# Kernel tuning notes

Measured on AMD Instinct MI355X. Metric: run time of the kernel, lower is better.

The kernel has to match this reference:

```python
import jax, jax.numpy as jnp
import numpy as np

HEADS = 16
HEAD_DIM = 4  # attention_channels(64) // num_heads(16)


def setup_inputs() -> dict:
    key = jax.random.key(0)
    ks = jax.random.split(key, 9)
    C, AC = 256, 64
    N, H, W = 1, 64, 64
    s_in = 1.0 / np.sqrt(C)
    s_out = 1.0 / np.sqrt(AC)
    return {
        "X":  jax.random.normal(ks[0], (N, C, H, W), jnp.float32),
        "Wq": jax.random.normal(ks[1], (AC, C), jnp.float32) * s_in,
        "bq": jax.random.normal(ks[2], (AC,), jnp.float32) * 0.01,
        "Wk": jax.random.normal(ks[3], (AC, C), jnp.float32) * s_in,
        "bk": jax.random.normal(ks[4], (AC,), jnp.float32) * 0.01,
        "Wv": jax.random.normal(ks[5], (AC, C), jnp.float32) * s_in,
        "bv": jax.random.normal(ks[6], (AC,), jnp.float32) * 0.01,
        "Wo": jax.random.normal(ks[7], (C, AC), jnp.float32) * s_out,
        "bo": jax.random.normal(ks[8], (C,), jnp.float32) * 0.01,
    }


def _l2norm_over_dim(x, eps=1e-12):
    # torch F.normalize(dim=-2): x / max(||x||_2, eps) along head-dim axis
    n = jnp.sqrt(jnp.sum(x * x, axis=-2, keepdims=True))
    return x / jnp.maximum(n, eps)


def reference(X, Wq, bq, Wk, bk, Wv, bv, Wo, bo):
    N, C, H, W = X.shape
    L = H * W
    def proj(Wm, bm):
        # 1x1 conv == channel matmul; reshape to (N, heads, d, L)
        y = jnp.einsum('oc,nchw->nohw', Wm, X) + bm[None, :, None, None]
        return y.reshape(N, HEADS, HEAD_DIM, L)
    Q = _l2norm_over_dim(proj(Wq, bq))
    K = _l2norm_over_dim(proj(Wk, bk))
    V = proj(Wv, bv)
    # attention_weights[l, m] = q_l . k_m, softmax over m (rows)
    A = jax.nn.softmax(jnp.einsum('nhdl,nhdm->nhlm', Q, K), axis=-1)
    # faithful to original: out = V @ A  -> out[d, i] = sum_j V[d, j] * A[j, i]
    out = jnp.einsum('nhdj,nhji->nhdi', V, A)
    out = out.reshape(N, HEADS * HEAD_DIM, H, W)
    out = jnp.einsum('co,nohw->nchw', Wo, out) + bo[None, :, None, None]
    return out + X
```

## Files before the change

### kernel.cpp

```cpp
#include <hip/hip_runtime.h>
#include <math.h>


constexpr int SL = 4096;
constexpr int NF = 126;

__device__ __forceinline__ float invfact(int e) {
    return e < 2 ? 1.f : e == 2 ? 0.5f : e == 3 ? (1.f / 6.f)
         : e == 4 ? (1.f / 24.f) : (1.f / 120.f);
}
__device__ __forceinline__ void f2abcd(int f, int& A, int& B, int& C, int& D) {
    for (int a = 0; a <= 5; ++a)
        for (int b = 0; b <= 5 - a; ++b)
            for (int c = 0; c <= 5 - a - b; ++c)
                for (int d = 0; d <= 5 - a - b - c; ++d)
                    if (f-- == 0) { A = a; B = b; C = c; D = d; return; }
}

#define FOR_MONOMIALS(BODY)                         \
    {                                               \
        int f = 0;                                  \
        _Pragma("unroll")                           \
        for (int a = 0; a <= 5; ++a)                \
        _Pragma("unroll")                           \
        for (int b = 0; b <= 5 - a; ++b)            \
        _Pragma("unroll")                           \
        for (int c = 0; c <= 5 - a - b; ++c)        \
        _Pragma("unroll")                           \
        for (int d = 0; d <= 5 - a - b - c; ++d) {  \
            BODY;                                   \
            ++f;                                    \
        }                                           \
    }

#define BUILD_POWERS(q)                                   \
    float p0[6], p1[6], p2[6], p3[6];                     \
    p0[0] = p1[0] = p2[0] = p3[0] = 1.f;                  \
    _Pragma("unroll")                                     \
    for (int t_ = 1; t_ < 6; ++t_) {                      \
        p0[t_] = p0[t_ - 1] * (q).x; p1[t_] = p1[t_ - 1] * (q).y; \
        p2[t_] = p2[t_ - 1] * (q).z; p3[t_] = p3[t_ - 1] * (q).w; }

__global__ __launch_bounds__(256) void qkv_kernel(
    const float* __restrict__ X,
    const float* __restrict__ Wq, const float* __restrict__ bq,
    const float* __restrict__ Wk, const float* __restrict__ bk,
    const float* __restrict__ Wv, const float* __restrict__ bv,
    float* __restrict__ Qn, float* __restrict__ Kn, float* __restrict__ V4)
{
    const int tid  = threadIdx.x;
    const int lane = tid & 63;
    const int wv   = __builtin_amdgcn_readfirstlane(tid >> 6);
    const int lt   = blockIdx.x;
    const int rb   = blockIdx.y;
    const int type = rb >> 2;
    const int rit  = (rb & 3) * 16 + wv * 4;
    const int l    = lt * 64 + lane;

    const float* W = type == 0 ? Wq : type == 1 ? Wk : Wv;
    const float* B = type == 0 ? bq : type == 1 ? bk : bv;
    const float* w0 = W + (rit + 0) * 256;
    const float* w1 = W + (rit + 1) * 256;
    const float* w2 = W + (rit + 2) * 256;
    const float* w3 = W + (rit + 3) * 256;

    float y0 = B[rit + 0], y1 = B[rit + 1], y2 = B[rit + 2], y3 = B[rit + 3];
    const float* Xl = X + l;
    #pragma unroll 8
    for (int c = 0; c < 256; ++c) {
        float x = Xl[c * SL];
        y0 = fmaf(w0[c], x, y0);
        y1 = fmaf(w1[c], x, y1);
        y2 = fmaf(w2[c], x, y2);
        y3 = fmaf(w3[c], x, y3);
    }
    if (type < 2) {
        float n = sqrtf(y0*y0 + y1*y1 + y2*y2 + y3*y3);
        float inv = 1.f / fmaxf(n, 1e-12f);
        y0 *= inv; y1 *= inv; y2 *= inv; y3 *= inv;
    }
    const int h = rit >> 2;
    float* base = type == 0 ? Qn : type == 1 ? Kn : V4;
    ((float4*)base)[h * SL + l] = make_float4(y0, y1, y2, y3);
}

template <int FC>
__device__ __forceinline__ void psi_accum(int h, int jc, int tid,
        const float* __restrict__ Kn, float acc[8])
{
    for (int u = 0; u < 4; ++u) {
        int j = jc * 1024 + u * 256 + tid;
        float4 k = ((const float4*)Kn)[h * SL + j];
        BUILD_POWERS(k)
        FOR_MONOMIALS({
            if (f >= FC * 8 && f < FC * 8 + 8)
                acc[f - FC * 8] += (p0[a] * p1[b]) * (p2[c] * p3[d]);
        })
    }
}

__global__ __launch_bounds__(256) void ssum_kernel(
    const float* __restrict__ Kn, float* __restrict__ Sp)
{
    const int tid = threadIdx.x;
    const int fc  = blockIdx.x;
    const int h   = blockIdx.y;
    const int jc  = blockIdx.z;
    float acc[8];
    #pragma unroll
    for (int k = 0; k < 8; ++k) acc[k] = 0.f;
    switch (fc) {
        case 0:  psi_accum<0 >(h, jc, tid, Kn, acc); break;
        case 1:  psi_accum<1 >(h, jc, tid, Kn, acc); break;
        case 2:  psi_accum<2 >(h, jc, tid, Kn, acc); break;
        case 3:  psi_accum<3 >(h, jc, tid, Kn, acc); break;
        case 4:  psi_accum<4 >(h, jc, tid, Kn, acc); break;
        case 5:  psi_accum<5 >(h, jc, tid, Kn, acc); break;
        case 6:  psi_accum<6 >(h, jc, tid, Kn, acc); break;
        case 7:  psi_accum<7 >(h, jc, tid, Kn, acc); break;
        case 8:  psi_accum<8 >(h, jc, tid, Kn, acc); break;
        case 9:  psi_accum<9 >(h, jc, tid, Kn, acc); break;
        case 10: psi_accum<10>(h, jc, tid, Kn, acc); break;
        case 11: psi_accum<11>(h, jc, tid, Kn, acc); break;
        case 12: psi_accum<12>(h, jc, tid, Kn, acc); break;
        case 13: psi_accum<13>(h, jc, tid, Kn, acc); break;
        case 14: psi_accum<14>(h, jc, tid, Kn, acc); break;
        default: psi_accum<15>(h, jc, tid, Kn, acc); break;
    }
    #pragma unroll
    for (int off = 32; off; off >>= 1)
        #pragma unroll
        for (int k = 0; k < 8; ++k) acc[k] += __shfl_down(acc[k], off);
    __shared__ float red[4][8];
    const int lane = tid & 63, wv = tid >> 6;
    if (lane == 0) {
        #pragma unroll
        for (int k = 0; k < 8; ++k) red[wv][k] = acc[k];
    }
    __syncthreads();
    if (tid < 8) {
        int f = fc * 8 + tid;
        if (f < NF) {
            float s = (red[0][tid] + red[1][tid]) + (red[2][tid] + red[3][tid]);
            int A, B, C, D; f2abcd(f, A, B, C, D);
            Sp[(jc * 16 + h) * 128 + f] =
                s * ((invfact(A) * invfact(B)) * (invfact(C) * invfact(D)));
        }
    }
}

__global__ __launch_bounds__(256) void zvz_kernel(
    const float* __restrict__ Qn, const float* __restrict__ Sp,
    const float* __restrict__ V4, float* __restrict__ Vz)
{
    __shared__ float Sf[128];
    const int tid = threadIdx.x;
    const int h   = blockIdx.y;
    if (tid < 128) {
        float s = 0.f;
        #pragma unroll
        for (int jc = 0; jc < 4; ++jc) s += Sp[(jc * 16 + h) * 128 + tid];
        Sf[tid] = s;
    }
    __syncthreads();
    const int j = blockIdx.x * 256 + tid;
    float4 q = ((const float4*)Qn)[h * SL + j];
    BUILD_POWERS(q)
    float z = 0.f;
    FOR_MONOMIALS({ z = fmaf((p0[a]*p1[b])*(p2[c]*p3[d]), Sf[f], z); })
    float inv = 1.f / z;
    float4 v = ((const float4*)V4)[h * SL + j];
    ((float4*)Vz)[h * SL + j] = make_float4(v.x*inv, v.y*inv, v.z*inv, v.w*inv);
}

template <int FC>
__device__ __forceinline__ void m_accum(int h, int jc, int tid,
        const float* __restrict__ Qn, const float* __restrict__ Vz,
        float acc[32])
{
    for (int u = 0; u < 4; ++u) {
        int j = jc * 1024 + u * 256 + tid;
        float4 q = ((const float4*)Qn)[h * SL + j];
        float4 v = ((const float4*)Vz)[h * SL + j];
        BUILD_POWERS(q)
        FOR_MONOMIALS({
            if (f >= FC * 8 && f < FC * 8 + 8) {
                const int fi = f - FC * 8;
                float m = (p0[a] * p1[b]) * (p2[c] * p3[d]);
                acc[fi*4+0] = fmaf(m, v.x, acc[fi*4+0]);
                acc[fi*4+1] = fmaf(m, v.y, acc[fi*4+1]);
                acc[fi*4+2] = fmaf(m, v.z, acc[fi*4+2]);
                acc[fi*4+3] = fmaf(m, v.w, acc[fi*4+3]);
            }
        })
    }
}

__global__ __launch_bounds__(256) void mmat_kernel(
    const float* __restrict__ Qn, const float* __restrict__ Vz,
    float* __restrict__ Mp)
{
    const int tid = threadIdx.x;
    const int fc  = blockIdx.x;
    const int h   = blockIdx.y;
    const int jc  = blockIdx.z;
    float acc[32];
    #pragma unroll
    for (int k = 0; k < 32; ++k) acc[k] = 0.f;
    switch (fc) {
        case 0:  m_accum<0 >(h, jc, tid, Qn, Vz, acc); break;
        case 1:  m_accum<1 >(h, jc, tid, Qn, Vz, acc); break;
        case 2:  m_accum<2 >(h, jc, tid, Qn, Vz, acc); break;
        case 3:  m_accum<3 >(h, jc, tid, Qn, Vz, acc); break;
        case 4:  m_accum<4 >(h, jc, tid, Qn, Vz, acc); break;
        case 5:  m_accum<5 >(h, jc, tid, Qn, Vz, acc); break;
        case 6:  m_accum<6 >(h, jc, tid, Qn, Vz, acc); break;
        case 7:  m_accum<7 >(h, jc, tid, Qn, Vz, acc); break;
        case 8:  m_accum<8 >(h, jc, tid, Qn, Vz, acc); break;
        case 9:  m_accum<9 >(h, jc, tid, Qn, Vz, acc); break;
        case 10: m_accum<10>(h, jc, tid, Qn, Vz, acc); break;
        case 11: m_accum<11>(h, jc, tid, Qn, Vz, acc); break;
        case 12: m_accum<12>(h, jc, tid, Qn, Vz, acc); break;
        case 13: m_accum<13>(h, jc, tid, Qn, Vz, acc); break;
        case 14: m_accum<14>(h, jc, tid, Qn, Vz, acc); break;
        default: m_accum<15>(h, jc, tid, Qn, Vz, acc); break;
    }
    #pragma unroll
    for (int off = 32; off; off >>= 1)
        #pragma unroll
        for (int k = 0; k < 32; ++k) acc[k] += __shfl_down(acc[k], off);
    __shared__ float red[4][32];
    const int lane = tid & 63, wv = tid >> 6;
    if (lane == 0) {
        #pragma unroll
        for (int k = 0; k < 32; ++k) red[wv][k] = acc[k];
    }
    __syncthreads();
    if (tid < 32) {
        int fi = tid >> 2, dd = tid & 3;
        int f = fc * 8 + fi;
        if (f < NF) {
            float s = (red[0][tid] + red[1][tid]) + (red[2][tid] + red[3][tid]);
            int A, B, C, D; f2abcd(f, A, B, C, D);
            s *= (invfact(A) * invfact(B)) * (invfact(C) * invfact(D));
            Mp[((jc * 16 + h) * 128 + f) * 4 + dd] = s;
        }
    }
}

template <int FC>
__device__ __forceinline__ void ao_accum(
        const float p0[6], const float p1[6], const float p2[6],
        const float p3[6], const float4* __restrict__ Mc, float acc[4])
{
    FOR_MONOMIALS({
        if (f >= FC * 32 && f < FC * 32 + 32 && f < NF) {
            float m = (p0[a] * p1[b]) * (p2[c] * p3[d]);
            float4 mm = Mc[f - FC * 32];
            acc[0] = fmaf(m, mm.x, acc[0]); acc[1] = fmaf(m, mm.y, acc[1]);
            acc[2] = fmaf(m, mm.z, acc[2]); acc[3] = fmaf(m, mm.w, acc[3]);
        }
    })
}

__global__ __launch_bounds__(256) void ao_kernel(
    const float* __restrict__ Kn, const float* __restrict__ Mp,
    float* __restrict__ AOp)
{
    __shared__ __align__(16) float Mc[32 * 4];
    const int tid = threadIdx.x;
    const int h   = blockIdx.y;
    const int fc  = blockIdx.z;
    const int nfl = (fc == 3) ? 30 : 32;
    if (tid < nfl * 4) {
        int fi = tid >> 2, dd = tid & 3;
        int f = fc * 32 + fi;
        float s = 0.f;
        #pragma unroll
        for (int jc = 0; jc < 4; ++jc)
            s += Mp[((jc * 16 + h) * 128 + f) * 4 + dd];
        Mc[fi * 4 + dd] = s;
    } else if (tid < 128) {
        Mc[tid] = 0.f;
    }
    __syncthreads();

    const int i = blockIdx.x * 256 + tid;
    float4 k = ((const float4*)Kn)[h * SL + i];
    BUILD_POWERS(k)
    float acc[4] = {0.f, 0.f, 0.f, 0.f};
    switch (fc) {
        case 0:  ao_accum<0>(p0, p1, p2, p3, (const float4*)Mc, acc); break;
        case 1:  ao_accum<1>(p0, p1, p2, p3, (const float4*)Mc, acc); break;
        case 2:  ao_accum<2>(p0, p1, p2, p3, (const float4*)Mc, acc); break;
        default: ao_accum<3>(p0, p1, p2, p3, (const float4*)Mc, acc); break;
    }
    float* A = AOp + (size_t)fc * 64 * SL;
    A[(h * 4 + 0) * SL + i] = acc[0];
    A[(h * 4 + 1) * SL + i] = acc[1];
    A[(h * 4 + 2) * SL + i] = acc[2];
    A[(h * 4 + 3) * SL + i] = acc[3];
}

__global__ __launch_bounds__(256) void oproj_kernel(
    const float* __restrict__ AOp, const float* __restrict__ Wo,
    const float* __restrict__ bo, const float* __restrict__ X,
    float* __restrict__ Y)
{
    const int lane = threadIdx.x & 63;
    const int wv   = __builtin_amdgcn_readfirstlane(threadIdx.x >> 6);
    const int i    = blockIdx.x * 64 + lane;
    const int cb   = blockIdx.y * 16 + wv * 4;

    float a0 = 0.f, a1 = 0.f, a2 = 0.f, a3 = 0.f;
    #pragma unroll 8
    for (int o = 0; o < 64; ++o) {
        float x = (AOp[o * SL + i] + AOp[262144 + o * SL + i])
                + (AOp[524288 + o * SL + i] + AOp[786432 + o * SL + i]);
        a0 = fmaf(Wo[(cb + 0) * 64 + o], x, a0);
        a1 = fmaf(Wo[(cb + 1) * 64 + o], x, a1);
        a2 = fmaf(Wo[(cb + 2) * 64 + o], x, a2);
        a3 = fmaf(Wo[(cb + 3) * 64 + o], x, a3);
    }
    Y[(cb + 0) * SL + i] = a0 + bo[cb + 0] + X[(cb + 0) * SL + i];
    Y[(cb + 1) * SL + i] = a1 + bo[cb + 1] + X[(cb + 1) * SL + i];
    Y[(cb + 2) * SL + i] = a2 + bo[cb + 2] + X[(cb + 2) * SL + i];
    Y[(cb + 3) * SL + i] = a3 + bo[cb + 3] + X[(cb + 3) * SL + i];
}

extern "C" void kernel_launch(void* const* d_in, const int* in_sizes, int n_in,
                              void* d_out, int out_size, void* d_ws, size_t ws_size,
                              hipStream_t stream)
{
    const float* X  = (const float*)d_in[0];
    const float* Wq = (const float*)d_in[1];
    const float* bq = (const float*)d_in[2];
    const float* Wk = (const float*)d_in[3];
    const float* bk = (const float*)d_in[4];
    const float* Wv = (const float*)d_in[5];
    const float* bv = (const float*)d_in[6];
    const float* Wo = (const float*)d_in[7];
    const float* bo = (const float*)d_in[8];
    float* Y = (float*)d_out;

    char* w = (char*)d_ws;
    float* Qn  = (float*)(w + (0 << 20));
    float* Kn  = (float*)(w + (1 << 20));
    float* V4  = (float*)(w + (2 << 20));
    float* Vz  = (float*)(w + (3 << 20));
    float* AOp = (float*)(w + (4 << 20));
    float* Sp  = (float*)(w + (8 << 20));
    float* Mp  = (float*)(w + (8 << 20) + (128 << 10));

    qkv_kernel<<<dim3(64, 12), 256, 0, stream>>>(X, Wq, bq, Wk, bk, Wv, bv,
                                                 Qn, Kn, V4);
    ssum_kernel<<<dim3(16, 16, 4), 256, 0, stream>>>(Kn, Sp);
    zvz_kernel<<<dim3(16, 16), 256, 0, stream>>>(Qn, Sp, V4, Vz);
    mmat_kernel<<<dim3(16, 16, 4), 256, 0, stream>>>(Qn, Vz, Mp);
    ao_kernel<<<dim3(16, 16, 4), 256, 0, stream>>>(Kn, Mp, AOp);
    oproj_kernel<<<dim3(64, 16), 256, 0, stream>>>(AOp, Wo, bo, X, Y);
}
```

Baseline: 126.4 us.

## Fuse attention-output evaluation with output projection and halve mmat j-chunks

Replaces the separate ao_kernel (four partial monomial chunks written to global AOp) and oproj_kernel with one fused kernel. Each block sums the Mp partials into shared memory, evaluates all 126 monomials per key position for every head, keeps the attention output tile in LDS, and applies the Wo projection plus bias and residual directly. mmat now splits the sequence into 2 chunks instead of 4, so there are fewer partials to reduce. This removes the large AOp global round trip and one launch. In exchange, each outfuse block redoes the full Mp reduction (32 KB of LDS) and the monomial evaluation is repeated across the 4 channel-block columns, with fewer blocks for mmat.

New measurement: 121.9 us, median of 2. 1.04x faster.

```diff
diff --git a/kernel.cpp b/kernel.cpp
--- a/kernel.cpp
+++ b/kernel.cpp
@@ -178,8 +178,8 @@
         const float* __restrict__ Qn, const float* __restrict__ Vz,
         float acc[32])
 {
-    for (int u = 0; u < 4; ++u) {
-        int j = jc * 1024 + u * 256 + tid;
+    for (int u = 0; u < 8; ++u) {
+        int j = jc * 2048 + u * 256 + tid;
         float4 q = ((const float4*)Qn)[h * SL + j];
         float4 v = ((const float4*)Vz)[h * SL + j];
         BUILD_POWERS(q)
@@ -248,84 +248,74 @@
     }
 }
 
-template <int FC>
-__device__ __forceinline__ void ao_accum(
-        const float p0[6], const float p1[6], const float p2[6],
-        const float p3[6], const float4* __restrict__ Mc, float acc[4])
-{
-    FOR_MONOMIALS({
-        if (f >= FC * 32 && f < FC * 32 + 32 && f < NF) {
+__global__ __launch_bounds__(256) void outfuse_kernel(
+    const float* __restrict__ Kn, const float* __restrict__ Mp,
+    const float* __restrict__ Wo, const float* __restrict__ bo,
+    const float* __restrict__ X, float* __restrict__ Y)
+{
+    __shared__ __align__(16) float ML[16 * 128 * 4];
+    __shared__ float AOL[64 * 33];
+    const int tid = threadIdx.x;
+    const int it  = blockIdx.x;
+    const int cb  = blockIdx.y;
+    const int i0  = it * 32;
+
+    {
+        const float4* Mp4 = (const float4*)Mp;
+        float4* ML4 = (float4*)ML;
+        #pragma unroll
+        for (int w = 0; w < 8; ++w) {
+            int e = tid + w * 256;
+            float4 a = Mp4[e], b = Mp4[2048 + e];
+            ML4[e] = make_float4(a.x+b.x, a.y+b.y, a.z+b.z, a.w+b.w);
+        }
+    }
+    __syncthreads();
+
+    #pragma unroll
+    for (int r = 0; r < 2; ++r) {
+        int p = tid + r * 256;
+        int pos = p & 31, h = p >> 5;
+        float4 k = ((const float4*)Kn)[h * SL + i0 + pos];
+        BUILD_POWERS(k)
+        const float4* Mh = ((const float4*)ML) + h * 128;
+        float a0 = 0.f, a1 = 0.f, a2 = 0.f, a3 = 0.f;
+        FOR_MONOMIALS({
             float m = (p0[a] * p1[b]) * (p2[c] * p3[d]);
-            float4 mm = Mc[f - FC * 32];
-            acc[0] = fmaf(m, mm.x, acc[0]); acc[1] = fmaf(m, mm.y, acc[1]);
-            acc[2] = fmaf(m, mm.z, acc[2]); acc[3] = fmaf(m, mm.w, acc[3]);
+            float4 mm = Mh[f];
+            a0 = fmaf(m, mm.x, a0); a1 = fmaf(m, mm.y, a1);
+            a2 = fmaf(m, mm.z, a2); a3 = fmaf(m, mm.w, a3);
+        })
+        AOL[(h * 4 + 0) * 33 + pos] = a0;
+        AOL[(h * 4 + 1) * 33 + pos] = a1;
+        AOL[(h * 4 + 2) * 33 + pos] = a2;
+        AOL[(h * 4 + 3) * 33 + pos] = a3;
+    }
+    __syncthreads();
+
+    const int pos = tid & 31, cg = tid >> 5;
+    const int chb = cb * 64 + cg * 8;
+    float acc[8];
+    #pragma unroll
+    for (int u = 0; u < 8; ++u) acc[u] = 0.f;
+    #pragma unroll 4
+    for (int ob = 0; ob < 16; ++ob) {
+        float x0 = AOL[(ob * 4 + 0) * 33 + pos];
+        float x1 = AOL[(ob * 4 + 1) * 33 + pos];
+        float x2 = AOL[(ob * 4 + 2) * 33 + pos];
+        float x3 = AOL[(ob * 4 + 3) * 33 + pos];
+        #pragma unroll
+        for (int u = 0; u < 8; ++u) {
+            float4 w4 = ((const float4*)Wo)[(chb + u) * 16 + ob];
+            acc[u] = fmaf(w4.x, x0, fmaf(w4.y, x1,
+                     fmaf(w4.z, x2, fmaf(w4.w, x3, acc[u]))));
         }
-    })
-}
-
-__global__ __launch_bounds__(256) void ao_kernel(
-    const float* __restrict__ Kn, const float* __restrict__ Mp,
-    float* __restrict__ AOp)
-{
-    __shared__ __align__(16) float Mc[32 * 4];
-    const int tid = threadIdx.x;
-    const int h   = blockIdx.y;
-    const int fc  = blockIdx.z;
-    const int nfl = (fc == 3) ? 30 : 32;
-    if (tid < nfl * 4) {
-        int fi = tid >> 2, dd = tid & 3;
-        int f = fc * 32 + fi;
-        float s = 0.f;
-        #pragma unroll
-        for (int jc = 0; jc < 4; ++jc)
-            s += Mp[((jc * 16 + h) * 128 + f) * 4 + dd];
-        Mc[fi * 4 + dd] = s;
-    } else if (tid < 128) {
-        Mc[tid] = 0.f;
-    }
-    __syncthreads();
-
-    const int i = blockIdx.x * 256 + tid;
-    float4 k = ((const float4*)Kn)[h * SL + i];
-    BUILD_POWERS(k)
-    float acc[4] = {0.f, 0.f, 0.f, 0.f};
-    switch (fc) {
-        case 0:  ao_accum<0>(p0, p1, p2, p3, (const float4*)Mc, acc); break;
-        case 1:  ao_accum<1>(p0, p1, p2, p3, (const float4*)Mc, acc); break;
-        case 2:  ao_accum<2>(p0, p1, p2, p3, (const float4*)Mc, acc); break;
-        default: ao_accum<3>(p0, p1, p2, p3, (const float4*)Mc, acc); break;
-    }
-    float* A = AOp + (size_t)fc * 64 * SL;
-    A[(h * 4 + 0) * SL + i] = acc[0];
-    A[(h * 4 + 1) * SL + i] = acc[1];
-    A[(h * 4 + 2) * SL + i] = acc[2];
-    A[(h * 4 + 3) * SL + i] = acc[3];
-}
-
-__global__ __launch_bounds__(256) void oproj_kernel(
-    const float* __restrict__ AOp, const float* __restrict__ Wo,
-    const float* __restrict__ bo, const float* __restrict__ X,
-    float* __restrict__ Y)
-{
-    const int lane = threadIdx.x & 63;
-    const int wv   = __builtin_amdgcn_readfirstlane(threadIdx.x >> 6);
-    const int i    = blockIdx.x * 64 + lane;
-    const int cb   = blockIdx.y * 16 + wv * 4;
-
-    float a0 = 0.f, a1 = 0.f, a2 = 0.f, a3 = 0.f;
-    #pragma unroll 8
-    for (int o = 0; o < 64; ++o) {
-        float x = (AOp[o * SL + i] + AOp[262144 + o * SL + i])
-                + (AOp[524288 + o * SL + i] + AOp[786432 + o * SL + i]);
-        a0 = fmaf(Wo[(cb + 0) * 64 + o], x, a0);
-        a1 = fmaf(Wo[(cb + 1) * 64 + o], x, a1);
-        a2 = fmaf(Wo[(cb + 2) * 64 + o], x, a2);
-        a3 = fmaf(Wo[(cb + 3) * 64 + o], x, a3);
-    }
-    Y[(cb + 0) * SL + i] = a0 + bo[cb + 0] + X[(cb + 0) * SL + i];
-    Y[(cb + 1) * SL + i] = a1 + bo[cb + 1] + X[(cb + 1) * SL + i];
-    Y[(cb + 2) * SL + i] = a2 + bo[cb + 2] + X[(cb + 2) * SL + i];
-    Y[(cb + 3) * SL + i] = a3 + bo[cb + 3] + X[(cb + 3) * SL + i];
+    }
+    #pragma unroll
+    for (int u = 0; u < 8; ++u) {
+        int ch = chb + u;
+        Y[ch * SL + i0 + pos] = acc[u] + bo[ch] + X[ch * SL + i0 + pos];
+    }
 }
 
 extern "C" void kernel_launch(void* const* d_in, const int* in_sizes, int n_in,
@@ -344,19 +334,17 @@
     float* Y = (float*)d_out;
 
     char* w = (char*)d_ws;
-    float* Qn  = (float*)(w + (0 << 20));
-    float* Kn  = (float*)(w + (1 << 20));
-    float* V4  = (float*)(w + (2 << 20));
-    float* Vz  = (float*)(w + (3 << 20));
-    float* AOp = (float*)(w + (4 << 20));
-    float* Sp  = (float*)(w + (8 << 20));
-    float* Mp  = (float*)(w + (8 << 20) + (128 << 10));
+    float* Qn = (float*)(w + (0 << 20));
+    float* Kn = (float*)(w + (1 << 20));
+    float* V4 = (float*)(w + (2 << 20));
+    float* Vz = (float*)(w + (3 << 20));
+    float* Sp = (float*)(w + (4 << 20));
+    float* Mp = (float*)(w + (4 << 20) + (128 << 10));
 
     qkv_kernel<<<dim3(64, 12), 256, 0, stream>>>(X, Wq, bq, Wk, bk, Wv, bv,
                                                  Qn, Kn, V4);
     ssum_kernel<<<dim3(16, 16, 4), 256, 0, stream>>>(Kn, Sp);
     zvz_kernel<<<dim3(16, 16), 256, 0, stream>>>(Qn, Sp, V4, Vz);
-    mmat_kernel<<<dim3(16, 16, 4), 256, 0, stream>>>(Qn, Vz, Mp);
-    ao_kernel<<<dim3(16, 16, 4), 256, 0, stream>>>(Kn, Mp, AOp);
-    oproj_kernel<<<dim3(64, 16), 256, 0, stream>>>(AOp, Wo, bo, X, Y);
-}
+    mmat_kernel<<<dim3(16, 16, 2), 256, 0, stream>>>(Qn, Vz, Mp);
+    outfuse_kernel<<<dim3(128, 4), 256, 0, stream>>>(Kn, Mp, Wo, bo, X, Y);
+}
```
